# Kernel optimization log

Measured on AMD Instinct MI355X. Metric: run time of the kernel, lower is better.

Reference implementation:

```python
import jax, jax.numpy as jnp
import numpy as np

BINS = 64


def _histogram(x, bins=BINS):
    """Faithful jax version of ColorHistogramLoss.get_histogram.

    Original semantics: edges = linspace(-1, 1, bins); bin j (j < bins-1) counts
    edges[j] <= v < edges[j+1]; last bin counts v >= edges[-1] (= 1).
    Values v < -1 fall in no bin. Single bucketize + scatter-add pass.
    """
    B, C = x.shape[0], x.shape[1]
    xf = x.reshape(B * C, -1)            # [B*C, N]
    N = xf.shape[1]
    edges = jnp.linspace(-1.0, 1.0, bins).astype(x.dtype)
    # searchsorted(side='right') - 1 gives j with edges[j] <= v < edges[j+1];
    # v < -1 -> -1 (invalid); v >= 1 -> bins-1 after clip (matches open last bin).
    idx = jnp.searchsorted(edges, xf, side='right') - 1
    valid = idx >= 0
    idx = jnp.clip(idx, 0, bins - 1)
    seg = idx + jnp.arange(B * C)[:, None] * bins      # per-(batch,channel) offset
    counts = jax.ops.segment_sum(
        valid.astype(jnp.float32).ravel(), seg.ravel(),
        num_segments=B * C * bins)
    return counts.reshape(B, C * bins) / N             # [B, C*bins]


def setup_inputs() -> dict:
    key = jax.random.key(0)
    k1, k2 = jax.random.split(key)
    shape = (32, 3, 512, 512)
    # pixels normalized to [-1, 1), matching the linspace(-1, 1) bin edges
    inp = jax.random.uniform(k1, shape, dtype=jnp.float32) * 2.0 - 1.0
    tgt = jax.random.uniform(k2, shape, dtype=jnp.float32) * 2.0 - 1.0
    return {"input": inp, "target": tgt}


def reference(input, target):
    hist_in = _histogram(input, BINS)
    hist_tgt = _histogram(target, BINS)
    return jnp.mean(jnp.abs(hist_in - hist_tgt))   # F.l1_loss (mean reduction)
```

## Files before the change

kernel.cpp:

```cpp
#include <hip/hip_runtime.h>


#define BINS 64
#define PLANES 96
#define PLANE_F4 65536
#define SEGS 32
#define SEG_F4 2048
#define TPB 256
#define F4T 8

struct Inv {
    unsigned long long b0, b1, b2, b3, b4, b5;
};

__device__ __forceinline__ int count_elem(float v, const Inv& iv) {
    int bin = (int)floorf((v + 1.0f) * 31.5f);
    int cb  = bin > 63 ? 63 : bin;
    unsigned long long m = __ballot(bin >= 0);
    m &= __ballot(cb & 1)  ^ iv.b0;
    m &= __ballot(cb & 2)  ^ iv.b1;
    m &= __ballot(cb & 4)  ^ iv.b2;
    m &= __ballot(cb & 8)  ^ iv.b3;
    m &= __ballot(cb & 16) ^ iv.b4;
    m &= __ballot(cb & 32) ^ iv.b5;
    return __popcll(m);
}

__device__ __forceinline__ int count4(float4 a, const Inv& iv) {
    return count_elem(a.x, iv) + count_elem(a.y, iv)
         + count_elem(a.z, iv) + count_elem(a.w, iv);
}

__global__ __launch_bounds__(TPB) void hist_diff_kernel(
        const float4* __restrict__ in4, const float4* __restrict__ tg4,
        int* __restrict__ gdiff) {
    const int tid  = threadIdx.x;
    const int lane = tid & 63;

    Inv iv;
    iv.b0 = (lane & 1)  ? 0ULL : ~0ULL;
    iv.b1 = (lane & 2)  ? 0ULL : ~0ULL;
    iv.b2 = (lane & 4)  ? 0ULL : ~0ULL;
    iv.b3 = (lane & 8)  ? 0ULL : ~0ULL;
    iv.b4 = (lane & 16) ? 0ULL : ~0ULL;
    iv.b5 = (lane & 32) ? 0ULL : ~0ULL;

    const int plane = blockIdx.x >> 5;
    const int seg   = blockIdx.x & (SEGS - 1);
    const long base = (long)plane * PLANE_F4 + (long)seg * SEG_F4 + tid;

    int acc = 0;

    float4 cur = in4[base];
#pragma unroll
    for (int k = 0; k < F4T; ++k) {
        float4 nxt = (k + 1 < F4T) ? in4[base + (k + 1) * TPB] : tg4[base];
        acc += count4(cur, iv);
        cur = nxt;
    }
#pragma unroll
    for (int k = 0; k < F4T; ++k) {
        float4 nxt = (k + 1 < F4T) ? tg4[base + (k + 1) * TPB]
                                   : make_float4(-2.f, -2.f, -2.f, -2.f);
        acc -= count4(cur, iv);
        cur = nxt;
    }

    __shared__ int lh[BINS];
    if (tid < BINS) lh[tid] = 0;
    __syncthreads();
    atomicAdd(&lh[lane], acc);
    __syncthreads();
    if (tid < BINS) {
        int v = lh[tid];
        if (v != 0) atomicAdd(&gdiff[plane * BINS + tid], v);
    }
}

__global__ __launch_bounds__(TPB) void reduce_abs_kernel(
        const int* __restrict__ gdiff, float* __restrict__ out) {
    int s = 0;
    for (int i = threadIdx.x; i < PLANES * BINS; i += TPB) {
        int v = gdiff[i];
        s += (v < 0) ? -v : v;
    }
#pragma unroll
    for (int off = 32; off > 0; off >>= 1) s += __shfl_down(s, off, 64);
    __shared__ int ws[TPB / 64];
    const int wid  = threadIdx.x >> 6;
    const int lane = threadIdx.x & 63;
    if (lane == 0) ws[wid] = s;
    __syncthreads();
    if (threadIdx.x == 0) {
        int total = 0;
#pragma unroll
        for (int w = 0; w < TPB / 64; ++w) total += ws[w];
        out[0] = (float)total * (1.0f / (262144.0f * 6144.0f));
    }
}

extern "C" void kernel_launch(void* const* d_in, const int* in_sizes, int n_in,
                              void* d_out, int out_size, void* d_ws, size_t ws_size,
                              hipStream_t stream) {
    const float4* inp = (const float4*)d_in[0];
    const float4* tgt = (const float4*)d_in[1];
    int* gdiff = (int*)d_ws;

    hipMemsetAsync(gdiff, 0, PLANES * BINS * sizeof(int), stream);
    hist_diff_kernel<<<PLANES * SEGS, TPB, 0, stream>>>(inp, tgt, gdiff);
    reduce_abs_kernel<<<1, TPB, 0, stream>>>(gdiff, (float*)d_out);
}
```

Before: 258.9 us.

## Replace ballot-based bin counting with per-thread private LDS histograms

Swaps the wavefront-ballot counting (six ballots plus a popcount per element per bin lane) for a private 16-bit histogram column per thread in shared memory, indexed directly by the bin, with an extra row that absorbs values below -1. All global loads are issued up front into registers, and a final pass sums each bin row across threads with packed 16-bit adds before one global atomic per bin per wave. This aims to cut ALU and ballot work per element. In exchange it uses about 33KB of LDS per block, which lowers occupancy, and the per-element shared read-modify-writes may hit bank conflicts.

```diff
diff --git a/kernel.cpp b/kernel.cpp
--- a/kernel.cpp
+++ b/kernel.cpp
@@ -8,72 +8,75 @@
 #define SEG_F4 2048
 #define TPB 256
 #define F4T 8
+#define NROWS 65
+#define LDS_U32 (NROWS * 256 * 2 / 4)
 
-struct Inv {
-    unsigned long long b0, b1, b2, b3, b4, b5;
-};
+typedef short short2v __attribute__((ext_vector_type(2)));
 
-__device__ __forceinline__ int count_elem(float v, const Inv& iv) {
-    int bin = (int)floorf((v + 1.0f) * 31.5f);
-    int cb  = bin > 63 ? 63 : bin;
-    unsigned long long m = __ballot(bin >= 0);
-    m &= __ballot(cb & 1)  ^ iv.b0;
-    m &= __ballot(cb & 2)  ^ iv.b1;
-    m &= __ballot(cb & 4)  ^ iv.b2;
-    m &= __ballot(cb & 8)  ^ iv.b3;
-    m &= __ballot(cb & 16) ^ iv.b4;
-    m &= __ballot(cb & 32) ^ iv.b5;
-    return __popcll(m);
-}
-
-__device__ __forceinline__ int count4(float4 a, const Inv& iv) {
-    return count_elem(a.x, iv) + count_elem(a.y, iv)
-         + count_elem(a.z, iv) + count_elem(a.w, iv);
+__device__ __forceinline__ void bump(unsigned short* __restrict__ col, float v, int delta) {
+    int bin = (int)((v + 1.0f) * 31.5f);
+    bin = bin > 63 ? 63 : bin;
+    int row = (v < -1.0f) ? 64 : bin;
+    col[row * 256] = (unsigned short)(col[row * 256] + delta);
 }
 
 __global__ __launch_bounds__(TPB) void hist_diff_kernel(
         const float4* __restrict__ in4, const float4* __restrict__ tg4,
         int* __restrict__ gdiff) {
+    __shared__ __align__(16) unsigned short hist[NROWS][256];
+
     const int tid  = threadIdx.x;
     const int lane = tid & 63;
+    const int wid  = tid >> 6;
 
-    Inv iv;
-    iv.b0 = (lane & 1)  ? 0ULL : ~0ULL;
-    iv.b1 = (lane & 2)  ? 0ULL : ~0ULL;
-    iv.b2 = (lane & 4)  ? 0ULL : ~0ULL;
-    iv.b3 = (lane & 8)  ? 0ULL : ~0ULL;
-    iv.b4 = (lane & 16) ? 0ULL : ~0ULL;
-    iv.b5 = (lane & 32) ? 0ULL : ~0ULL;
+    {
+        uint4* p = (uint4*)&hist[0][0];
+#pragma unroll
+        for (int i = 0; i < 9; ++i) {
+            int idx = tid + i * TPB;
+            if (idx < LDS_U32 / 4) p[idx] = make_uint4(0, 0, 0, 0);
+        }
+    }
+    __syncthreads();
 
     const int plane = blockIdx.x >> 5;
     const int seg   = blockIdx.x & (SEGS - 1);
     const long base = (long)plane * PLANE_F4 + (long)seg * SEG_F4 + tid;
 
-    int acc = 0;
+    float4 a[F4T], b[F4T];
+#pragma unroll
+    for (int k = 0; k < F4T; ++k) a[k] = in4[base + k * TPB];
+#pragma unroll
+    for (int k = 0; k < F4T; ++k) b[k] = tg4[base + k * TPB];
 
-    float4 cur = in4[base];
+    unsigned short* col = &hist[0][tid];
 #pragma unroll
     for (int k = 0; k < F4T; ++k) {
-        float4 nxt = (k + 1 < F4T) ? in4[base + (k + 1) * TPB] : tg4[base];
-        acc += count4(cur, iv);
-        cur = nxt;
+        bump(col, a[k].x, 1); bump(col, a[k].y, 1);
+        bump(col, a[k].z, 1); bump(col, a[k].w, 1);
     }
 #pragma unroll
     for (int k = 0; k < F4T; ++k) {
-        float4 nxt = (k + 1 < F4T) ? tg4[base + (k + 1) * TPB]
-                                   : make_float4(-2.f, -2.f, -2.f, -2.f);
-        acc -= count4(cur, iv);
-        cur = nxt;
+        bump(col, b[k].x, -1); bump(col, b[k].y, -1);
+        bump(col, b[k].z, -1); bump(col, b[k].w, -1);
     }
+    __syncthreads();
 
-    __shared__ int lh[BINS];
-    if (tid < BINS) lh[tid] = 0;
-    __syncthreads();
-    atomicAdd(&lh[lane], acc);
-    __syncthreads();
-    if (tid < BINS) {
-        int v = lh[tid];
-        if (v != 0) atomicAdd(&gdiff[plane * BINS + tid], v);
+    {
+        const uint4* rowp = (const uint4*)&hist[lane][wid * 64];
+        short2v acc; acc.x = 0; acc.y = 0;
+#pragma unroll
+        for (int it = 0; it < 8; ++it) {
+            int j = (it + lane) & 7;
+            uint4 w4 = rowp[j];
+            union { uint4 u; short2v s2[4]; } cv; cv.u = w4;
+            acc = acc + cv.s2[0];
+            acc = acc + cv.s2[1];
+            acc = acc + cv.s2[2];
+            acc = acc + cv.s2[3];
+        }
+        int s = (int)acc.x + (int)acc.y;
+        if (s != 0) atomicAdd(&gdiff[plane * BINS + lane], s);
     }
 }
 
```

After: 214.8 us. -17.0%, faster.
